# Kernel tuning notes

Hardware: AMD Instinct MI355X
Metric: run time of the kernel (lower is better)

## Reference

```python
import jax, jax.numpy as jnp
import numpy as np

K = 3
STRIDE = 1
PAD = 1
C_IN = 128
C_OUT = 128
B, H, W = 4, 128, 128


def conv2d(x, w, b, stride, pad):
    # x: (B,C,H,W), w: (O,I,kh,kw)
    out = jax.lax.conv_general_dilated(
        x, w, window_strides=(stride, stride),
        padding=[(pad, pad), (pad, pad)],
        dimension_numbers=("NCHW", "OIHW", "NCHW"))
    return out + b[None, :, None, None]


def bilinear_sample(img, ix, iy):
    # img: (C,H,W); ix, iy: (N,) float pixel coords.
    # Bilinear, padding_mode='zeros', align_corners=False semantics.
    C, Hc, Wc = img.shape
    x0 = jnp.floor(ix).astype(jnp.int32)
    y0 = jnp.floor(iy).astype(jnp.int32)
    x1 = x0 + 1
    y1 = y0 + 1
    wx1 = ix - x0.astype(img.dtype)
    wy1 = iy - y0.astype(img.dtype)
    wx0 = 1.0 - wx1
    wy0 = 1.0 - wy1

    def gather(yi, xi):
        valid = ((yi >= 0) & (yi < Hc) & (xi >= 0) & (xi < Wc)).astype(img.dtype)
        v = img[:, jnp.clip(yi, 0, Hc - 1), jnp.clip(xi, 0, Wc - 1)]  # (C,N)
        return v * valid[None, :]

    return (gather(y0, x0) * (wy0 * wx0)[None]
            + gather(y0, x1) * (wy0 * wx1)[None]
            + gather(y1, x0) * (wy1 * wx0)[None]
            + gather(y1, x1) * (wy1 * wx1)[None])


def setup_inputs() -> dict:
    key = jax.random.key(0)
    k1, k2, k3 = jax.random.split(key, 3)
    x = jax.random.normal(k1, (B, C_IN, H, W), dtype=jnp.float32)
    # offset conv: small random so grid_sample does real irregular gathers
    w_off = jax.random.normal(k2, (2 * K * K, C_IN, K, K), dtype=jnp.float32) * 0.01
    b_off = jnp.zeros((2 * K * K,), dtype=jnp.float32)
    # main conv: kaiming normal, fan_out = C_OUT*K*K
    std = float(np.sqrt(2.0 / (C_OUT * K * K)))
    w_main = jax.random.normal(k3, (C_OUT, C_IN, K, K), dtype=jnp.float32) * std
    b_main = jnp.zeros((C_OUT,), dtype=jnp.float32)
    return {"x": x, "w_off": w_off, "b_off": b_off,
            "w_main": w_main, "b_main": b_main}


def reference(x, w_off, b_off, w_main, b_main):
    Bx, C, Hx, Wx = x.shape
    off = conv2d(x, w_off, b_off, STRIDE, PAD)        # (B, 2*K*K, Ho, Wo)
    Ho, Wo = off.shape[2], off.shape[3]
    off = off.transpose(0, 2, 3, 1).reshape(Bx, Ho, Wo, K, K, 2)
    # snake cumulative offsets: x-offset cumsum over kernel row i, y over col j
    off_x = jnp.cumsum(off[..., 0], axis=3)           # over first kernel dim
    off_y = jnp.cumsum(off[..., 1], axis=4)           # over second kernel dim
    off = jnp.stack([off_x, off_y], axis=-1).reshape(Bx, Ho, Wo, K * K, 2)

    yr = jnp.linspace(-1.0, 1.0, Ho, dtype=x.dtype)
    xr = jnp.linspace(-1.0, 1.0, Wo, dtype=x.dtype)
    yg, xg = jnp.meshgrid(yr, xr, indexing="ij")
    base = jnp.stack([xg, yg], axis=-1)[None, :, :, None, :]  # (1,Ho,Wo,1,2)
    grid = (base + off).reshape(Bx, -1, 2)            # (B, Ho*Wo*K*K, 2)

    # unnormalize (align_corners=False)
    ix = ((grid[..., 0] + 1.0) * Wx - 1.0) * 0.5
    iy = ((grid[..., 1] + 1.0) * Hx - 1.0) * 0.5
    sampled = jax.vmap(bilinear_sample)(x, ix, iy)    # (B, C, Ho*Wo*K*K)
    sampled = sampled.reshape(Bx, C, Ho, Wo, K * K)

    w = w_main.reshape(w_main.shape[0], C, K * K)     # (O, C, K*K)
    out = jnp.einsum("bchwk,ock->bohw", sampled, w)
    return out + b_main[None, :, None, None]
```

## Files before the change

kernel.cpp:

```cpp
#include <hip/hip_runtime.h>
#include <cstddef>

#define Bb   4
#define CI   128
#define CO   128
#define Hh   128
#define Ww   128
#define HW   (Hh*Ww)
#define NOFF 18
#define NTAP 9
#define KTOT (NTAP*CI)
#define NSTEP 36

typedef short short8 __attribute__((ext_vector_type(8)));
typedef _Float16 half8 __attribute__((ext_vector_type(8)));
typedef float floatx4 __attribute__((ext_vector_type(4)));

__device__ inline unsigned short bf16_rne_bits(float f) {
    unsigned u = __float_as_uint(f);
    unsigned r = u + 0x7FFFu + ((u >> 16) & 1u);
    return (unsigned short)(r >> 16);
}
__device__ inline float bf16_bits_to_f32(unsigned short h) {
    return __uint_as_float((unsigned)h << 16);
}
__device__ inline unsigned short f32_to_f16_bits(float f) {
    union { _Float16 h; unsigned short u; } cv;
    cv.h = (_Float16)f;
    return cv.u;
}

__global__ __launch_bounds__(256) void k_transpose(const float* __restrict__ x,
                                                   _Float16* __restrict__ xt16,
                                                   unsigned short* __restrict__ xbh,
                                                   unsigned short* __restrict__ xbl) {
    __shared__ float tile[32][33];
    int b  = blockIdx.z;
    int c0 = blockIdx.y * 32;
    int p0 = blockIdx.x * 32;
    int tx = threadIdx.x;
    int ty = threadIdx.y;
    const float* xb = x + (size_t)b * CI * HW;
    size_t obase = (size_t)b * HW * CI;
#pragma unroll
    for (int i = 0; i < 4; ++i) {
        int c = c0 + ty + 8 * i;
        tile[ty + 8 * i][tx] = xb[(size_t)c * HW + p0 + tx];
    }
    __syncthreads();
#pragma unroll
    for (int i = 0; i < 4; ++i) {
        int p = p0 + ty + 8 * i;
        float v = tile[tx][ty + 8 * i];
        size_t o = obase + (size_t)p * CI + c0 + tx;
        xt16[o] = (_Float16)v;
        unsigned short hb = bf16_rne_bits(v);
        xbh[o] = hb;
        xbl[o] = bf16_rne_bits(v - bf16_bits_to_f32(hb));
    }
}

__global__ __launch_bounds__(256) void k_weights(const float* __restrict__ w_off,
                                                 const float* __restrict__ w_main,
                                                 unsigned short* __restrict__ wofh,
                                                 unsigned short* __restrict__ wofl,
                                                 unsigned short* __restrict__ wf16) {
    int idx = blockIdx.x * 256 + threadIdx.x;
    int stride = gridDim.x * 256;
    for (int i = idx; i < 9 * 4 * 2 * 512; i += stride) {
        int j  = i & 7;
        int l  = (i >> 3) & 63;
        int nt = (i >> 9) & 1;
        int ks = (i >> 10) & 3;
        int t  = i >> 12;
        int oc = nt * 16 + (l & 15);
        int c  = ks * 32 + (l >> 4) * 8 + j;
        float f = (oc < NOFF) ? w_off[(oc * CI + c) * 9 + t] : 0.f;
        unsigned short hb = bf16_rne_bits(f);
        wofh[i] = hb;
        wofl[i] = bf16_rne_bits(f - bf16_bits_to_f32(hb));
    }
    for (int i = idx; i < CO * KTOT; i += stride) {
        int j  = i & 7;
        int l  = (i >> 3) & 63;
        int g  = (i >> 9) & 7;
        int ks = (i >> 12) & 3;
        int t  = i >> 14;
        int o  = g * 16 + (l & 15);
        int c  = ks * 32 + (l >> 4) * 8 + j;
        wf16[i] = f32_to_f16_bits(w_main[(o * CI + c) * 9 + t]);
    }
}

__global__ __launch_bounds__(256, 2) void k_offsets(const unsigned short* __restrict__ xbh,
                                                    const unsigned short* __restrict__ xbl,
                                                    const unsigned short* __restrict__ wofh,
                                                    const unsigned short* __restrict__ wofl,
                                                    const float* __restrict__ b_off,
                                                    float2* __restrict__ coords) {
    __shared__ __align__(16) unsigned short ph[3 * 34 * 128];
    __shared__ __align__(16) unsigned short pl[3 * 34 * 128];
    __shared__ float raw[32][19];
    int blk = blockIdx.x;
    int wt  = blk & 3;
    int h   = (blk >> 2) & 127;
    int b   = blk >> 9;
    int w0  = wt * 32;
    int tid  = threadIdx.x;
    int lane = tid & 63;
    int wave = tid >> 6;

    size_t xb0 = (size_t)b * HW * CI;
    for (int i = tid; i < 3 * 34 * 64; i += 256) {
        int c2  = i & 63;
        int col = (i >> 6) % 34;
        int r   = i / (34 * 64);
        int gy  = h - 1 + r;
        int gx  = w0 - 1 + col;
        unsigned vh = 0, vl = 0;
        if (gy >= 0 && gy < Hh && gx >= 0 && gx < Ww) {
            size_t o = xb0 + ((size_t)gy * Ww + gx) * CI + c2 * 2;
            vh = *(const unsigned*)(xbh + o);
            vl = *(const unsigned*)(xbl + o);
        }
        int byte = (((r * 34 + col) * 128) + c2 * 2) * 2;
        byte ^= (col & 7) << 4;
        *(unsigned*)((char*)ph + byte) = vh;
        *(unsigned*)((char*)pl + byte) = vl;
    }
    __syncthreads();

    int m   = wave & 1;
    int nt  = wave >> 1;
    int l15 = lane & 15, lhi = lane >> 4;
    floatx4 accE = (floatx4){0.f, 0.f, 0.f, 0.f};
    floatx4 accO = (floatx4){0.f, 0.f, 0.f, 0.f};
    const short8* bhp = (const short8*)wofh;
    const short8* blp = (const short8*)wofl;
#pragma unroll
    for (int t = 0; t < 9; ++t) {
        int ki = t / 3, kj = t % 3;
        int colb = m * 16 + l15 + kj;
        int rowoff = (ki * 34 + colb) * 256;
#pragma unroll
        for (int ks = 0; ks < 4; ++ks) {
            int abyte = (rowoff + ks * 64 + lhi * 16) ^ ((colb & 7) << 4);
            short8 Ah = *(const short8*)((char*)ph + abyte);
            short8 Al = *(const short8*)((char*)pl + abyte);
            size_t bi = (size_t)((t * 4 + ks) * 2 + nt) * 64 + lane;
            short8 Bh = bhp[bi];
            short8 Bl = blp[bi];
            floatx4& a = (ks & 1) ? accO : accE;
            a = __builtin_amdgcn_mfma_f32_16x16x32_bf16(Ah, Bh, a, 0, 0, 0);
            a = __builtin_amdgcn_mfma_f32_16x16x32_bf16(Ah, Bl, a, 0, 0, 0);
            a = __builtin_amdgcn_mfma_f32_16x16x32_bf16(Al, Bh, a, 0, 0, 0);
        }
    }
    int oc = nt * 16 + l15;
    if (oc < NOFF) {
        float bo = b_off[oc];
#pragma unroll
        for (int r = 0; r < 4; ++r) {
            int px = m * 16 + lhi * 4 + r;
            raw[px][oc] = (accE[r] + accO[r]) + bo;
        }
    }
    __syncthreads();

    for (int i = tid; i < 32 * NTAP; i += 256) {
        int px = i / NTAP;
        int t  = i % NTAP;
        int ki = t / 3, kj = t % 3;
        float offx = 0.f, offy = 0.f;
        for (int q = 0; q <= ki; ++q) offx += raw[px][q * 6 + kj * 2 + 0];
        for (int q = 0; q <= kj; ++q) offy += raw[px][ki * 6 + q * 2 + 1];
        int wg = w0 + px;
        float xg = -1.0f + 2.0f * (float)wg / 127.0f;
        float yg = -1.0f + 2.0f * (float)h  / 127.0f;
        float gxn = xg + offx;
        float gyn = yg + offy;
        float ix = ((gxn + 1.0f) * (float)Ww - 1.0f) * 0.5f;
        float iy = ((gyn + 1.0f) * (float)Hh - 1.0f) * 0.5f;
        coords[(((size_t)b * Hh + h) * Ww + wg) * NTAP + t] = make_float2(ix, iy);
    }
}

__global__ __launch_bounds__(256) void k_sample(const _Float16* __restrict__ xt16,
                                                const float2* __restrict__ coords,
                                                unsigned short* __restrict__ af16,
                                                int q0) {
    int nb = gridDim.x;
    int blkid = blockIdx.x;
    int cpx = nb >> 3;
    blkid = (blkid & 7) * cpx + (blkid >> 3);
    int task = blkid * 4 + (threadIdx.x >> 6);
    int lane = threadIdx.x & 63;
    int Pl   = task / 9;
    int tap  = task - Pl * 9;
    int r = lane & 15, q = lane >> 4;
    int p = q0 + Pl * 16 + r;
    int b = p >> 14;

    float2 co = coords[(size_t)p * NTAP + tap];
    float ix = co.x, iy = co.y;
    float fx0 = floorf(ix), fy0 = floorf(iy);
    int x0 = (int)fx0, y0 = (int)fy0;
    int x1 = x0 + 1,   y1 = y0 + 1;
    float wx1 = ix - fx0, wy1 = iy - fy0;
    float wx0 = 1.f - wx1, wy0 = 1.f - wy1;
    bool vx0 = (x0 >= 0) & (x0 < Ww);
    bool vx1 = (x1 >= 0) & (x1 < Ww);
    bool vy0 = (y0 >= 0) & (y0 < Hh);
    bool vy1 = (y1 >= 0) & (y1 < Hh);
    int cx0 = min(max(x0, 0), Ww - 1), cx1 = min(max(x1, 0), Ww - 1);
    int cy0 = min(max(y0, 0), Hh - 1), cy1 = min(max(y1, 0), Hh - 1);
    float w00 = (vy0 && vx0) ? wy0 * wx0 : 0.f;
    float w01 = (vy0 && vx1) ? wy0 * wx1 : 0.f;
    float w10 = (vy1 && vx0) ? wy1 * wx0 : 0.f;
    float w11 = (vy1 && vx1) ? wy1 * wx1 : 0.f;

    const _Float16* xb  = xt16 + (size_t)b * HW * CI + q * 8;
    const _Float16* r00 = xb + ((size_t)cy0 * Ww + cx0) * CI;
    const _Float16* r01 = xb + ((size_t)cy0 * Ww + cx1) * CI;
    const _Float16* r10 = xb + ((size_t)cy1 * Ww + cx0) * CI;
    const _Float16* r11 = xb + ((size_t)cy1 * Ww + cx1) * CI;
    size_t obase = ((size_t)(Pl * 36 + tap * 4) * 64 + lane) * 8;

#pragma unroll
    for (int ks = 0; ks < 4; ++ks) {
        int c = ks * 32;
        half8 a8 = *(const half8*)(r00 + c);
        half8 b8 = *(const half8*)(r01 + c);
        half8 c8 = *(const half8*)(r10 + c);
        half8 d8 = *(const half8*)(r11 + c);
        short8 hv;
#pragma unroll
        for (int j = 0; j < 8; ++j) {
            float v = w00 * (float)a8[j] + w01 * (float)b8[j]
                    + w10 * (float)c8[j] + w11 * (float)d8[j];
            hv[j] = (short)f32_to_f16_bits(v);
        }
        *(short8*)(af16 + obase + (size_t)ks * 512) = hv;
    }
}

__global__ __launch_bounds__(256, 4) void k_gemm(const unsigned short* __restrict__ af16,
                                                 const unsigned short* __restrict__ wf16,
                                                 const float* __restrict__ b_main,
                                                 float* __restrict__ out, int q0) {
    __shared__ __align__(16) float epi[CO * 33];
    int nb = gridDim.x;
    int cpx = nb >> 3;
    int blk = blockIdx.x;
    blk = (blk & 7) * cpx + (blk >> 3);
    int tid = threadIdx.x, lane = tid & 63, wave = tid >> 6;
    int wave_n = wave & 1, wave_m = wave >> 1;
    int l15 = lane & 15, lhi = lane >> 4;
    int P = blk * 2 + wave_m;

    const half8* ah = (const half8*)af16 + (size_t)P * NSTEP * 64 + lane;
    const half8* bh = (const half8*)wf16 + (size_t)wave_n * 4 * 64 + lane;

    floatx4 acc[4];
#pragma unroll
    for (int n = 0; n < 4; ++n) acc[n] = (floatx4){0.f, 0.f, 0.f, 0.f};

    half8 A0, B0[4], A1, B1[4];
    A0 = ah[0];
#pragma unroll
    for (int n = 0; n < 4; ++n) B0[n] = bh[(size_t)n * 64];

#pragma unroll 2
    for (int s = 0; s < NSTEP; s += 2) {
        A1 = ah[(size_t)(s + 1) * 64];
#pragma unroll
        for (int n = 0; n < 4; ++n) B1[n] = bh[(size_t)((s + 1) * 8 + n) * 64];
#pragma unroll
        for (int n = 0; n < 4; ++n)
            acc[n] = __builtin_amdgcn_mfma_f32_16x16x32_f16(A0, B0[n], acc[n], 0, 0, 0);
        if (s + 2 < NSTEP) {
            A0 = ah[(size_t)(s + 2) * 64];
#pragma unroll
            for (int n = 0; n < 4; ++n) B0[n] = bh[(size_t)((s + 2) * 8 + n) * 64];
        }
#pragma unroll
        for (int n = 0; n < 4; ++n)
            acc[n] = __builtin_amdgcn_mfma_f32_16x16x32_f16(A1, B1[n], acc[n], 0, 0, 0);
    }

#pragma unroll
    for (int n = 0; n < 4; ++n) {
        int o = wave_n * 64 + n * 16 + l15;
#pragma unroll
        for (int rr = 0; rr < 4; ++rr) {
            int px = wave_m * 16 + lhi * 4 + rr;
            epi[o * 33 + px] = acc[n][rr];
        }
    }
    __syncthreads();
    int p_blk = q0 + blk * 32;
    int b = p_blk >> 14, hw = p_blk & 16383;
    float* ob = out + (size_t)b * CO * HW + hw;
    for (int i = tid; i < CO * 32; i += 256) {
        int o  = i >> 5;
        int px = i & 31;
        __builtin_nontemporal_store(epi[o * 33 + px] + b_main[o],
                                    &ob[(size_t)o * HW + px]);
    }
}

extern "C" void kernel_launch(void* const* d_in, const int* in_sizes, int n_in,
                              void* d_out, int out_size, void* d_ws, size_t ws_size,
                              hipStream_t stream) {
    const float* x      = (const float*)d_in[0];
    const float* w_off  = (const float*)d_in[1];
    const float* b_off  = (const float*)d_in[2];
    const float* w_main = (const float*)d_in[3];
    const float* b_main = (const float*)d_in[4];
    float* out = (float*)d_out;

    char* base = (char*)d_ws;
    _Float16*       xt16 = (_Float16*)base;
    unsigned short* xbh  = (unsigned short*)(base + 16777216);
    unsigned short* xbl  = (unsigned short*)(base + 2 * 16777216);
    float2*         coords = (float2*)(base + 3 * 16777216);
    unsigned short* wofh = (unsigned short*)(base + 3 * 16777216 + 4718592);
    unsigned short* wofl = wofh + 9 * 4 * 2 * 512;
    unsigned short* wf16 = wofl + 9 * 4 * 2 * 512;
    size_t fixed_b = 3ull * 16777216 + 4718592
                   + 2 * (9 * 4 * 2 * 512) * 2 + (size_t)CO * KTOT * 2;
    unsigned short* af16 = (unsigned short*)(base + fixed_b);

    size_t avail = (ws_size > fixed_b) ? (ws_size - fixed_b) : 0;
    long long maxpx = (long long)(avail / 2304);
    int chunk = (int)((maxpx / 2048) * 2048);
    if (chunk > 32768) chunk = 32768;
    if (chunk < 2048) chunk = 2048;

    k_transpose<<<dim3(HW / 32, CI / 32, Bb), dim3(32, 8), 0, stream>>>(x, xt16, xbh, xbl);
    k_weights<<<576, 256, 0, stream>>>(w_off, w_main, wofh, wofl, wf16);
    k_offsets<<<Bb * Hh * (Ww / 32), 256, 0, stream>>>(xbh, xbl, wofh, wofl, b_off, coords);
    for (int q0 = 0; q0 < Bb * HW; q0 += chunk) {
        int np = Bb * HW - q0; if (np > chunk) np = chunk;
        k_sample<<<(np / 16) * 9 / 4, 256, 0, stream>>>(xt16, coords, af16, q0);
        k_gemm<<<np / 32, 256, 0, stream>>>(af16, wf16, b_main, out, q0);
    }
}
```

Baseline: 214.2 us.

## Split offset-conv taps across waves with half-width tiles and partial-sum reduction

The offset convolution kernel now handles 16-pixel tiles instead of 32, doubling the grid. Instead of splitting waves by pixel half, waves split the 9 kernel taps into two groups (4 and 5). Each group writes partial sums to shared memory, which are added during the cumsum step. This shortens each wave's serial MFMA chain and cuts shared memory per block to raise occupancy, at the cost of more redundant halo loads (18 columns for 16 pixels) and more blocks.

After: 189.5 us (median of 2 runs). 1.13x faster.

```diff
diff --git a/kernel.cpp b/kernel.cpp
--- a/kernel.cpp
+++ b/kernel.cpp
@@ -98,23 +98,23 @@
                                                     const unsigned short* __restrict__ wofl,
                                                     const float* __restrict__ b_off,
                                                     float2* __restrict__ coords) {
-    __shared__ __align__(16) unsigned short ph[3 * 34 * 128];
-    __shared__ __align__(16) unsigned short pl[3 * 34 * 128];
-    __shared__ float raw[32][19];
+    __shared__ __align__(16) unsigned short ph[3 * 18 * 128];
+    __shared__ __align__(16) unsigned short pl[3 * 18 * 128];
+    __shared__ float rawp[2][16][19];
     int blk = blockIdx.x;
-    int wt  = blk & 3;
-    int h   = (blk >> 2) & 127;
-    int b   = blk >> 9;
-    int w0  = wt * 32;
+    int wt  = blk & 7;
+    int h   = (blk >> 3) & 127;
+    int b   = blk >> 10;
+    int w0  = wt * 16;
     int tid  = threadIdx.x;
     int lane = tid & 63;
     int wave = tid >> 6;
 
     size_t xb0 = (size_t)b * HW * CI;
-    for (int i = tid; i < 3 * 34 * 64; i += 256) {
+    for (int i = tid; i < 3 * 18 * 64; i += 256) {
         int c2  = i & 63;
-        int col = (i >> 6) % 34;
-        int r   = i / (34 * 64);
+        int col = (i >> 6) % 18;
+        int r   = i / (18 * 64);
         int gy  = h - 1 + r;
         int gx  = w0 - 1 + col;
         unsigned vh = 0, vl = 0;
@@ -123,57 +123,71 @@
             vh = *(const unsigned*)(xbh + o);
             vl = *(const unsigned*)(xbl + o);
         }
-        int byte = (((r * 34 + col) * 128) + c2 * 2) * 2;
+        int byte = (((r * 18 + col) * 128) + c2 * 2) * 2;
         byte ^= (col & 7) << 4;
         *(unsigned*)((char*)ph + byte) = vh;
         *(unsigned*)((char*)pl + byte) = vl;
     }
     __syncthreads();
 
-    int m   = wave & 1;
-    int nt  = wave >> 1;
+    int nt  = wave & 1;
+    int th  = wave >> 1;
     int l15 = lane & 15, lhi = lane >> 4;
     floatx4 accE = (floatx4){0.f, 0.f, 0.f, 0.f};
     floatx4 accO = (floatx4){0.f, 0.f, 0.f, 0.f};
     const short8* bhp = (const short8*)wofh;
     const short8* blp = (const short8*)wofl;
-#pragma unroll
-    for (int t = 0; t < 9; ++t) {
-        int ki = t / 3, kj = t % 3;
-        int colb = m * 16 + l15 + kj;
-        int rowoff = (ki * 34 + colb) * 256;
-#pragma unroll
-        for (int ks = 0; ks < 4; ++ks) {
-            int abyte = (rowoff + ks * 64 + lhi * 16) ^ ((colb & 7) << 4);
-            short8 Ah = *(const short8*)((char*)ph + abyte);
-            short8 Al = *(const short8*)((char*)pl + abyte);
-            size_t bi = (size_t)((t * 4 + ks) * 2 + nt) * 64 + lane;
-            short8 Bh = bhp[bi];
-            short8 Bl = blp[bi];
-            floatx4& a = (ks & 1) ? accO : accE;
-            a = __builtin_amdgcn_mfma_f32_16x16x32_bf16(Ah, Bh, a, 0, 0, 0);
-            a = __builtin_amdgcn_mfma_f32_16x16x32_bf16(Ah, Bl, a, 0, 0, 0);
-            a = __builtin_amdgcn_mfma_f32_16x16x32_bf16(Al, Bh, a, 0, 0, 0);
-        }
-    }
+
+#define TAP_STEP(t)                                                              \
+    {                                                                            \
+        const int ki = (t) / 3, kj = (t) % 3;                                    \
+        int colb = l15 + kj;                                                     \
+        int rowoff = (ki * 18 + colb) * 256;                                     \
+        _Pragma("unroll")                                                        \
+        for (int ks = 0; ks < 4; ++ks) {                                         \
+            int abyte = (rowoff + ks * 64 + lhi * 16) ^ ((colb & 7) << 4);       \
+            short8 Ah = *(const short8*)((char*)ph + abyte);                     \
+            short8 Al = *(const short8*)((char*)pl + abyte);                     \
+            size_t bi = (size_t)(((t) * 4 + ks) * 2 + nt) * 64 + lane;           \
+            short8 Bh = bhp[bi];                                                 \
+            short8 Bl = blp[bi];                                                 \
+            floatx4& a = (ks & 1) ? accO : accE;                                 \
+            a = __builtin_amdgcn_mfma_f32_16x16x32_bf16(Ah, Bh, a, 0, 0, 0);     \
+            a = __builtin_amdgcn_mfma_f32_16x16x32_bf16(Ah, Bl, a, 0, 0, 0);     \
+            a = __builtin_amdgcn_mfma_f32_16x16x32_bf16(Al, Bh, a, 0, 0, 0);     \
+        }                                                                        \
+    }
+    if (th == 0) {
+        TAP_STEP(0) TAP_STEP(1) TAP_STEP(2) TAP_STEP(3)
+    } else {
+        TAP_STEP(4) TAP_STEP(5) TAP_STEP(6) TAP_STEP(7) TAP_STEP(8)
+    }
+#undef TAP_STEP
+
     int oc = nt * 16 + l15;
     if (oc < NOFF) {
-        float bo = b_off[oc];
+        float bo = (th == 0) ? b_off[oc] : 0.f;
 #pragma unroll
         for (int r = 0; r < 4; ++r) {
-            int px = m * 16 + lhi * 4 + r;
-            raw[px][oc] = (accE[r] + accO[r]) + bo;
+            int px = lhi * 4 + r;
+            rawp[th][px][oc] = (accE[r] + accO[r]) + bo;
         }
     }
     __syncthreads();
 
-    for (int i = tid; i < 32 * NTAP; i += 256) {
+    for (int i = tid; i < 16 * NTAP; i += 256) {
         int px = i / NTAP;
         int t  = i % NTAP;
         int ki = t / 3, kj = t % 3;
         float offx = 0.f, offy = 0.f;
-        for (int q = 0; q <= ki; ++q) offx += raw[px][q * 6 + kj * 2 + 0];
-        for (int q = 0; q <= kj; ++q) offy += raw[px][ki * 6 + q * 2 + 1];
+        for (int q = 0; q <= ki; ++q) {
+            int idx = q * 6 + kj * 2 + 0;
+            offx += rawp[0][px][idx] + rawp[1][px][idx];
+        }
+        for (int q = 0; q <= kj; ++q) {
+            int idx = ki * 6 + q * 2 + 1;
+            offy += rawp[0][px][idx] + rawp[1][px][idx];
+        }
         int wg = w0 + px;
         float xg = -1.0f + 2.0f * (float)wg / 127.0f;
         float yg = -1.0f + 2.0f * (float)h  / 127.0f;
@@ -339,7 +353,7 @@
 
     k_transpose<<<dim3(HW / 32, CI / 32, Bb), dim3(32, 8), 0, stream>>>(x, xt16, xbh, xbl);
     k_weights<<<576, 256, 0, stream>>>(w_off, w_main, wofh, wofl, wf16);
-    k_offsets<<<Bb * Hh * (Ww / 32), 256, 0, stream>>>(xbh, xbl, wofh, wofl, b_off, coords);
+    k_offsets<<<Bb * Hh * (Ww / 16), 256, 0, stream>>>(xbh, xbl, wofh, wofl, b_off, coords);
     for (int q0 = 0; q0 < Bb * HW; q0 += chunk) {
         int np = Bb * HW - q0; if (np > chunk) np = chunk;
         k_sample<<<(np / 16) * 9 / 4, 256, 0, stream>>>(xt16, coords, af16, q0);
```
